# Optimization experiments

Measured on AMD Instinct MI355X. Metric: run time of the kernel, lower is better.

The kernel has to match this reference:

```python
import jax, jax.numpy as jnp
import numpy as np

D_MODEL = 64
D_K = 64
N_HEADS = 4
D_FF = 64
LN_EPS = 1e-5


def _layernorm(x, g, b):
    mu = jnp.mean(x, axis=-1, keepdims=True)
    var = jnp.var(x, axis=-1, keepdims=True)
    return (x - mu) * jax.lax.rsqrt(var + LN_EPS) * g + b


def setup_inputs() -> dict:
    key = jax.random.key(0)
    ks = jax.random.split(key, 20)
    B, L = 8, 2048
    s = 0.05
    inp = {
        "x": jax.random.normal(ks[0], (B, L, D_MODEL), jnp.float32),
        "attn_mask": jax.random.randint(ks[1], (B, L, L), 0, 2).astype(bool),
        "u": jax.random.normal(ks[2], (B, 1, D_MODEL), jnp.float32),
        "wq": jax.random.normal(ks[3], (D_MODEL, D_K * N_HEADS), jnp.float32) * s,
        "wk": jax.random.normal(ks[4], (D_MODEL, D_K * N_HEADS), jnp.float32) * s,
        "wv": jax.random.normal(ks[5], (D_MODEL, D_K * N_HEADS), jnp.float32) * s,
        "uqw": jax.random.normal(ks[6], (D_MODEL, D_K), jnp.float32) * s,
        "ukw": jax.random.normal(ks[7], (D_MODEL, D_K), jnp.float32) * s,
        "uvw": jax.random.normal(ks[8], (D_MODEL, D_K), jnp.float32) * s,
        "sq1": jax.random.normal(ks[9], (D_MODEL, D_MODEL // 2), jnp.float32) * s,
        "sq2": jax.random.normal(ks[10], (D_MODEL // 2, 1), jnp.float32) * s,
        "sk1": jax.random.normal(ks[11], (D_MODEL, D_MODEL // 2), jnp.float32) * s,
        "sk2": jax.random.normal(ks[12], (D_MODEL // 2, 1), jnp.float32) * s,
        "sv1": jax.random.normal(ks[13], (D_MODEL, D_MODEL // 2), jnp.float32) * s,
        "sv2": jax.random.normal(ks[14], (D_MODEL // 2, 1), jnp.float32) * s,
        "fcw": jax.random.normal(ks[15], (N_HEADS * D_K, D_MODEL), jnp.float32) * s,
        "ln1_g": jnp.ones((D_MODEL,), jnp.float32),
        "ln1_b": jnp.zeros((D_MODEL,), jnp.float32),
        "ffn1": jax.random.normal(ks[16], (D_MODEL, D_FF), jnp.float32) * s,
        "ffn2": jax.random.normal(ks[17], (D_FF, D_MODEL), jnp.float32) * s,
        "ln2_g": jnp.ones((D_MODEL,), jnp.float32),
        "ln2_b": jnp.zeros((D_MODEL,), jnp.float32),
    }
    return inp


def reference(x, attn_mask, u, wq, wk, wv, uqw, ukw, uvw, sq1, sq2, sk1, sk2,
              sv1, sv2, fcw, ln1_g, ln1_b, ffn1, ffn2, ln2_g, ln2_b):
    B, L, _ = x.shape
    H, dk = N_HEADS, D_K
    # per-head Q,K,V: [B,H,L,dk]
    Q = (x @ wq).reshape(B, L, H, dk).transpose(0, 2, 1, 3)
    K = (x @ wk).reshape(B, L, H, dk).transpose(0, 2, 1, 3)
    V = (x @ wv).reshape(B, L, H, dk).transpose(0, 2, 1, 3)
    # broadcast scalar gates from u: [B,1,1]
    S_q = jax.nn.relu(u @ sq1) @ sq2
    S_k = jax.nn.relu(u @ sk1) @ sk2
    S_v = jax.nn.relu(u @ sv1) @ sv2
    uQ = (x @ uqw) * S_q  # [B,L,dk]
    uK = (x @ ukw) * S_k
    uV = (x @ uvw) * S_v
    scores = (jnp.einsum('bhqd,bhkd->bhqk', Q, K)
              + jnp.einsum('bqd,bkd->bqk', uQ, uK)[:, None]) / jnp.sqrt(
                  jnp.asarray(dk, x.dtype))
    scores = jnp.where(attn_mask[:, None], jnp.asarray(-1e9, x.dtype), scores)
    attn = jax.nn.softmax(scores, axis=-1)  # [B,H,L,L]
    ctx = jnp.einsum('bhqk,bhkd->bhqd', attn, V + uV[:, None])
    ctx = ctx.transpose(0, 2, 1, 3).reshape(B, L, H * dk)
    out = ctx @ fcw  # dropout is identity in eval mode
    enc = _layernorm(out + x, ln1_g, ln1_b)
    ffn = jax.nn.relu(enc @ ffn1) @ ffn2
    res = _layernorm(ffn + enc, ln2_g, ln2_b)
    return (res, attn)
```

## Files before the change

kernel.cpp:

```cpp
#include <hip/hip_runtime.h>
#include <hip/hip_bf16.h>
#include <stdint.h>

typedef __bf16  bf16x8  __attribute__((ext_vector_type(8)));
typedef float   f32x4   __attribute__((ext_vector_type(4)));
typedef unsigned short u16x8 __attribute__((ext_vector_type(8)));
typedef unsigned short ushort_t;

__device__ __forceinline__ unsigned short f2b(float f) {
    __hip_bfloat16 h = __float2bfloat16(f);
    return *reinterpret_cast<unsigned short*>(&h);
}

__device__ __forceinline__ void cp16(const void* g, void* l) {
    __builtin_amdgcn_global_load_lds(
        (const __attribute__((address_space(1))) unsigned int*)g,
        (__attribute__((address_space(3))) unsigned int*)l,
        16, 0, 0);
}

#define BB 8
#define LL 2048
#define DM 64
#define NH 4
#define DK 64

__global__ __launch_bounds__(256) void k_maskpack(const int* __restrict__ mask,
                                                  unsigned int* __restrict__ words) {
    int tid = blockIdx.x * 256 + threadIdx.x;
    const int4* p = reinterpret_cast<const int4*>(mask) + (size_t)tid * 8;
    unsigned int wbits = 0u;
    #pragma unroll
    for (int i = 0; i < 8; i++) {
        int4 v = p[i];
        wbits |= (v.x != 0 ? 1u << (4 * i + 0) : 0u);
        wbits |= (v.y != 0 ? 1u << (4 * i + 1) : 0u);
        wbits |= (v.z != 0 ? 1u << (4 * i + 2) : 0u);
        wbits |= (v.w != 0 ? 1u << (4 * i + 3) : 0u);
    }
    words[tid] = wbits;
}

__global__ __launch_bounds__(64) void k_gates(const float* __restrict__ u,
                                              const float* s1q, const float* s2q,
                                              const float* s1k, const float* s2k,
                                              const float* s1v, const float* s2v,
                                              float* __restrict__ gates) {
    int b = blockIdx.x, g = blockIdx.y, lane = threadIdx.x;
    const float* s1 = (g == 0) ? s1q : (g == 1) ? s1k : s1v;
    const float* s2 = (g == 0) ? s2q : (g == 1) ? s2k : s2v;
    float ur = u[b * 64 + lane];
    float acc = 0.f;
    for (int j = 0; j < 64; j++) {
        float uj = __shfl(ur, j, 64);
        if (lane < 32) acc += uj * s1[j * 32 + lane];
    }
    float r = (lane < 32) ? fmaxf(acc, 0.f) * s2[lane] : 0.f;
    for (int m = 32; m >= 1; m >>= 1) r += __shfl_xor(r, m, 64);
    if (lane == 0) gates[b * 3 + g] = r;
}

__global__ __launch_bounds__(256) void k_proj(const float* __restrict__ x,
                                              const float* __restrict__ wq,
                                              const float* __restrict__ wk,
                                              const float* __restrict__ wv,
                                              const float* __restrict__ uqw,
                                              const float* __restrict__ ukw,
                                              const float* __restrict__ uvw,
                                              const float* __restrict__ gates,
                                              ushort_t* __restrict__ Qe,
                                              ushort_t* __restrict__ Ke,
                                              ushort_t* __restrict__ VeT) {
    int lt = blockIdx.x, b = blockIdx.y, t = threadIdx.x;
    int l0 = lt * 32;
    __shared__ float lx[32][68];
    __shared__ float luv[32][68];
    #pragma unroll
    for (int i = 0; i < 2; i++) {
        int id = t + i * 256;
        int r = id >> 4, c4 = id & 15;
        float4 v = *(const float4*)&x[((b * LL) + l0 + r) * 64 + c4 * 4];
        *(float4*)&lx[r][c4 * 4] = v;
    }
    __syncthreads();
    float Sq = gates[b * 3 + 0], Sk = gates[b * 3 + 1], Sv = gates[b * 3 + 2];
    if (t < 192) {
        int m = t >> 6, d = t & 63;
        const float* uw = (m == 0) ? uqw : (m == 1) ? ukw : uvw;
        float acc[32];
        #pragma unroll
        for (int r = 0; r < 32; r++) acc[r] = 0.f;
        for (int j = 0; j < 64; j += 4) {
            float w0 = uw[(j + 0) * 64 + d], w1 = uw[(j + 1) * 64 + d];
            float w2 = uw[(j + 2) * 64 + d], w3 = uw[(j + 3) * 64 + d];
            #pragma unroll
            for (int r = 0; r < 32; r++) {
                float4 xv = *(const float4*)&lx[r][j];
                acc[r] += xv.x * w0 + xv.y * w1 + xv.z * w2 + xv.w * w3;
            }
        }
        if (m == 2) {
            #pragma unroll
            for (int r = 0; r < 32; r++) luv[r][d] = acc[r] * Sv;
        } else if (m == 0) {
            for (int r = 0; r < 32; r++) {
                unsigned short v = f2b(acc[r] * Sq * 0.125f);
                int base = ((b * NH) * LL + l0 + r) * 128 + 64 + d;
                #pragma unroll
                for (int hh2 = 0; hh2 < 4; hh2++) Qe[base + hh2 * (LL * 128)] = v;
            }
        } else {
            for (int r = 0; r < 32; r++) {
                unsigned short v = f2b(acc[r] * Sk);
                int col = 64 + (d ^ ((r & 7) << 3));
                int base = ((b * NH) * LL + l0 + r) * 128 + col;
                #pragma unroll
                for (int hh2 = 0; hh2 < 4; hh2++) Ke[base + hh2 * (LL * 128)] = v;
            }
        }
    }
    __syncthreads();
    int c = t, hh = c >> 6, d = c & 63;
    float aq_[32], ak_[32], av_[32];
    #pragma unroll
    for (int r = 0; r < 32; r++) { aq_[r] = 0.f; ak_[r] = 0.f; av_[r] = 0.f; }
    for (int j = 0; j < 64; j += 4) {
        float q0w = wq[(j + 0) * 256 + c], q1w = wq[(j + 1) * 256 + c];
        float q2w = wq[(j + 2) * 256 + c], q3w = wq[(j + 3) * 256 + c];
        float k0w = wk[(j + 0) * 256 + c], k1w = wk[(j + 1) * 256 + c];
        float k2w = wk[(j + 2) * 256 + c], k3w = wk[(j + 3) * 256 + c];
        float v0w = wv[(j + 0) * 256 + c], v1w = wv[(j + 1) * 256 + c];
        float v2w = wv[(j + 2) * 256 + c], v3w = wv[(j + 3) * 256 + c];
        #pragma unroll
        for (int r = 0; r < 32; r++) {
            float4 xv = *(const float4*)&lx[r][j];
            aq_[r] += xv.x * q0w + xv.y * q1w + xv.z * q2w + xv.w * q3w;
            ak_[r] += xv.x * k0w + xv.y * k1w + xv.z * k2w + xv.w * k3w;
            av_[r] += xv.x * v0w + xv.y * v1w + xv.z * v2w + xv.w * v3w;
        }
    }
    int outbase = (b * NH + hh) * LL + l0;
    #pragma unroll
    for (int r = 0; r < 32; r++) Qe[(outbase + r) * 128 + d] = f2b(aq_[r] * 0.125f);
    #pragma unroll
    for (int r = 0; r < 32; r++)
        Ke[(outbase + r) * 128 + (d ^ ((r & 7) << 3))] = f2b(ak_[r]);
    long vbase = ((long)(b * NH + hh) * 64 + d) * LL;
    int lblk = l0 & ~63, loff = l0 & 63;
    #pragma unroll
    for (int rb = 0; rb < 4; rb++) {
        u16x8 vv;
        #pragma unroll
        for (int k = 0; k < 8; k++) {
            int r = rb * 8 + k;
            vv[k] = f2b(av_[r] + luv[r][d]);
        }
        int off = (loff + rb * 8) ^ ((d & 7) << 3);
        *(u16x8*)&VeT[vbase + lblk + off] = vv;
    }
}

__global__ __launch_bounds__(256) void k_attn(const ushort_t* __restrict__ Qe,
                                              const ushort_t* __restrict__ Ke,
                                              const ushort_t* __restrict__ VeT,
                                              const unsigned int* __restrict__ mwords,
                                              float* __restrict__ ctx,
                                              float* __restrict__ attn) {
    int lin = blockIdx.x + 32 * blockIdx.y + 128 * blockIdx.z;
    int sw  = ((lin & 7) << 7) | (lin >> 3);
    int qt = sw & 31, h = (sw >> 5) & 3, b = sw >> 7;

    int t = threadIdx.x, w = t >> 6, lane = t & 63, quad = lane >> 4, l15 = lane & 15;
    int q0 = qt * 64;
    int bh = b * NH + h;
    const ushort_t* QeB = Qe + (long)bh * LL * 128;
    const ushort_t* KeB = Ke + (long)bh * LL * 128;
    const ushort_t* VtB = VeT + (long)bh * 64 * LL;
    float* attnB = attn + (long)bh * LL * LL;
    const unsigned int* mB = mwords + (long)(b * LL) * 64;

    __shared__ ushort_t sKe[2][64 * 128];
    __shared__ ushort_t sVT[2][64 * 64];
    __shared__ unsigned int smask[64][66];
    __shared__ ushort_t sPb[4][16][72];

    #pragma unroll
    for (int i = 0; i < 16; i++) {
        int id = t + i * 256;
        smask[id >> 6][id & 63] = mB[(q0 + (id >> 6)) * 64 + (id & 63)];
    }

    bf16x8 aq[4];
    int qrow = q0 + w * 16 + l15;
    #pragma unroll
    for (int c = 0; c < 4; c++)
        aq[c] = *(const bf16x8*)&QeB[qrow * 128 + c * 32 + quad * 8];

    int swz = (l15 & 7) << 3;
    int mrow = w * 16 + quad * 4;
    float lsum[4] = {0.f, 0.f, 0.f, 0.f};

    #pragma unroll
    for (int i = 0; i < 4; i++) {
        int off = (t + i * 256) * 16;
        cp16((const char*)KeB + off, (char*)&sKe[0][0] + off);
    }
    for (int kt = 0; kt < 32; kt++) {
        int cur = kt & 1;
        __syncthreads();
        if (kt < 31) {
            size_t gb = (size_t)(kt + 1) * 64 * 256;
            #pragma unroll
            for (int i = 0; i < 4; i++) {
                int off = (t + i * 256) * 16;
                cp16((const char*)KeB + gb + off, (char*)&sKe[cur ^ 1][0] + off);
            }
        }
        #pragma unroll
        for (int nb = 0; nb < 4; nb++) {
            f32x4 s = (f32x4){0.f, 0.f, 0.f, 0.f};
            #pragma unroll
            for (int c = 0; c < 4; c++) {
                bf16x8 kb = *(const bf16x8*)&sKe[cur][(nb * 16 + l15) * 128 + ((c * 32 + quad * 8) ^ swz)];
                s = __builtin_amdgcn_mfma_f32_16x16x32_bf16(aq[c], kb, s, 0, 0, 0);
            }
            #pragma unroll
            for (int reg = 0; reg < 4; reg++) {
                unsigned int word = smask[mrow + reg][kt * 2 + (nb >> 1)];
                unsigned int bit = (word >> ((nb & 1) * 16 + l15)) & 1u;
                lsum[reg] += bit ? 0.f : __expf(fminf(s[reg], 60.f));
            }
        }
    }
    float inv[4];
    #pragma unroll
    for (int reg = 0; reg < 4; reg++) {
        float v = lsum[reg];
        #pragma unroll
        for (int m = 1; m < 16; m <<= 1) v += __shfl_xor(v, m, 16);
        inv[reg] = (v > 0.f) ? 1.f / v : 0.f;
    }

    f32x4 cacc[4];
    #pragma unroll
    for (int db = 0; db < 4; db++) cacc[db] = (f32x4){0.f, 0.f, 0.f, 0.f};

    #pragma unroll
    for (int i = 0; i < 4; i++) {
        int off = (t + i * 256) * 16;
        cp16((const char*)KeB + off, (char*)&sKe[0][0] + off);
    }
    #pragma unroll
    for (int i = 0; i < 2; i++) {
        int off = (t + i * 256) * 16;
        int d = off >> 7, cb = off & 127;
        cp16((const char*)VtB + (size_t)d * (LL * 2) + cb, (char*)&sVT[0][0] + off);
    }
    for (int kt = 0; kt < 32; kt++) {
        int cur = kt & 1;
        int k0 = kt * 64;
        __syncthreads();
        if (kt < 31) {
            size_t gKe = (size_t)(k0 + 64) * 256;
            #pragma unroll
            for (int i = 0; i < 4; i++) {
                int off = (t + i * 256) * 16;
                cp16((const char*)KeB + gKe + off, (char*)&sKe[cur ^ 1][0] + off);
            }
            #pragma unroll
            for (int i = 0; i < 2; i++) {
                int off = (t + i * 256) * 16;
                int d = off >> 7, cb = off & 127;
                cp16((const char*)VtB + (size_t)d * (LL * 2) + (size_t)(k0 + 64) * 2 + cb,
                     (char*)&sVT[cur ^ 1][0] + off);
            }
        }
        #pragma unroll
        for (int nb = 0; nb < 4; nb++) {
            f32x4 s = (f32x4){0.f, 0.f, 0.f, 0.f};
            #pragma unroll
            for (int c = 0; c < 4; c++) {
                bf16x8 kb = *(const bf16x8*)&sKe[cur][(nb * 16 + l15) * 128 + ((c * 32 + quad * 8) ^ swz)];
                s = __builtin_amdgcn_mfma_f32_16x16x32_bf16(aq[c], kb, s, 0, 0, 0);
            }
            #pragma unroll
            for (int reg = 0; reg < 4; reg++) {
                unsigned int word = smask[mrow + reg][kt * 2 + (nb >> 1)];
                unsigned int bit = (word >> ((nb & 1) * 16 + l15)) & 1u;
                float p = bit ? 0.f : __expf(fminf(s[reg], 60.f));
                sPb[w][quad * 4 + reg][nb * 16 + l15] = f2b(p);
                __builtin_nontemporal_store(p * inv[reg],
                    &attnB[(long)(q0 + mrow + reg) * LL + k0 + nb * 16 + l15]);
            }
        }
        #pragma unroll
        for (int db = 0; db < 4; db++) {
            #pragma unroll
            for (int c2 = 0; c2 < 2; c2++) {
                bf16x8 a  = *(const bf16x8*)&sPb[w][l15][c2 * 32 + quad * 8];
                bf16x8 bb = *(const bf16x8*)&sVT[cur][(db * 16 + l15) * 64 + ((c2 * 32 + quad * 8) ^ swz)];
                cacc[db] = __builtin_amdgcn_mfma_f32_16x16x32_bf16(a, bb, cacc[db], 0, 0, 0);
            }
        }
    }
    #pragma unroll
    for (int db = 0; db < 4; db++)
        #pragma unroll
        for (int reg = 0; reg < 4; reg++) {
            int qr = q0 + mrow + reg;
            ctx[((long)(b * LL) + qr) * 256 + h * 64 + db * 16 + l15] = cacc[db][reg] * inv[reg];
        }
}

__global__ __launch_bounds__(256) void k_epi(const float* __restrict__ ctx,
                                             const float* __restrict__ x,
                                             const float* __restrict__ fcw,
                                             const float* __restrict__ g1,
                                             const float* __restrict__ b1,
                                             const float* __restrict__ f1,
                                             const float* __restrict__ f2,
                                             const float* __restrict__ g2,
                                             const float* __restrict__ b2w,
                                             float* __restrict__ res) {
    int w = threadIdx.x >> 6, lane = threadIdx.x & 63;
    int row = blockIdx.x * 4 + w;
    const float* cr = ctx + (long)row * 256;
    float creg[4];
    #pragma unroll
    for (int i = 0; i < 4; i++) creg[i] = cr[i * 64 + lane];
    float acc = 0.f;
    #pragma unroll
    for (int j = 0; j < 256; j++) {
        float cj = __shfl(creg[j >> 6], j & 63, 64);
        acc += cj * fcw[j * 64 + lane];
    }
    float val = acc + x[row * 64 + lane];
    float mu = val;
    #pragma unroll
    for (int m = 1; m < 64; m <<= 1) mu += __shfl_xor(mu, m, 64);
    mu *= (1.f / 64.f);
    float d0 = val - mu;
    float var = d0 * d0;
    #pragma unroll
    for (int m = 1; m < 64; m <<= 1) var += __shfl_xor(var, m, 64);
    var *= (1.f / 64.f);
    float enc = d0 * rsqrtf(var + 1e-5f) * g1[lane] + b1[lane];
    float a1 = 0.f;
    #pragma unroll
    for (int j = 0; j < 64; j++) a1 += __shfl(enc, j, 64) * f1[j * 64 + lane];
    float hrel = fmaxf(a1, 0.f);
    float a2 = 0.f;
    #pragma unroll
    for (int j = 0; j < 64; j++) a2 += __shfl(hrel, j, 64) * f2[j * 64 + lane];
    float v2 = a2 + enc;
    float mu2 = v2;
    #pragma unroll
    for (int m = 1; m < 64; m <<= 1) mu2 += __shfl_xor(mu2, m, 64);
    mu2 *= (1.f / 64.f);
    float d2 = v2 - mu2;
    float var2 = d2 * d2;
    #pragma unroll
    for (int m = 1; m < 64; m <<= 1) var2 += __shfl_xor(var2, m, 64);
    var2 *= (1.f / 64.f);
    float outv = d2 * rsqrtf(var2 + 1e-5f) * g2[lane] + b2w[lane];
    res[row * 64 + lane] = outv;
}

extern "C" void kernel_launch(void* const* d_in, const int* in_sizes, int n_in,
                              void* d_out, int out_size, void* d_ws, size_t ws_size,
                              hipStream_t stream) {
    const float* x    = (const float*)d_in[0];
    const int*   mask = (const int*)d_in[1];
    const float* u    = (const float*)d_in[2];
    const float* wq   = (const float*)d_in[3];
    const float* wk   = (const float*)d_in[4];
    const float* wv   = (const float*)d_in[5];
    const float* uqw  = (const float*)d_in[6];
    const float* ukw  = (const float*)d_in[7];
    const float* uvw  = (const float*)d_in[8];
    const float* sq1  = (const float*)d_in[9];
    const float* sq2  = (const float*)d_in[10];
    const float* sk1  = (const float*)d_in[11];
    const float* sk2  = (const float*)d_in[12];
    const float* sv1  = (const float*)d_in[13];
    const float* sv2  = (const float*)d_in[14];
    const float* fcw  = (const float*)d_in[15];
    const float* g1   = (const float*)d_in[16];
    const float* b1   = (const float*)d_in[17];
    const float* f1   = (const float*)d_in[18];
    const float* f2   = (const float*)d_in[19];
    const float* g2   = (const float*)d_in[20];
    const float* b2w  = (const float*)d_in[21];

    char* ws = (char*)d_ws;
    float*        gates  = (float*)(ws + 0);
    unsigned int* mwords = (unsigned int*)(ws + 4096);
    ushort_t*     Qe     = (ushort_t*)(ws + 4198400);
    ushort_t*     Ke     = (ushort_t*)(ws + 20975616);
    ushort_t*     VeT    = (ushort_t*)(ws + 37752832);
    float*        ctx    = (float*)(ws + 46141440);

    float* res  = (float*)d_out;
    float* attn = (float*)d_out + (size_t)BB * LL * DM;

    k_maskpack<<<dim3(4096), dim3(256), 0, stream>>>(mask, mwords);
    k_gates<<<dim3(8, 3), dim3(64), 0, stream>>>(u, sq1, sq2, sk1, sk2, sv1, sv2, gates);
    k_proj<<<dim3(64, 8), dim3(256), 0, stream>>>(x, wq, wk, wv, uqw, ukw, uvw, gates, Qe, Ke, VeT);
    k_attn<<<dim3(32, 4, 8), dim3(256), 0, stream>>>(Qe, Ke, VeT, mwords, ctx, attn);
    k_epi<<<dim3(4096), dim3(256), 0, stream>>>(ctx, x, fcw, g1, b1, f1, f2, g2, b2w, res);
}
```

Before: 1.006 ms.

## Split attention warps into 2x2 query/key tiles to reuse K fragments

```diff
diff --git a/kernel.cpp b/kernel.cpp
--- a/kernel.cpp
+++ b/kernel.cpp
@@ -171,6 +171,7 @@
     int qt = sw & 31, h = (sw >> 5) & 3, b = sw >> 7;
 
     int t = threadIdx.x, w = t >> 6, lane = t & 63, quad = lane >> 4, l15 = lane & 15;
+    int qh = w >> 1, kh = w & 1;
     int q0 = qt * 64;
     int bh = b * NH + h;
     const ushort_t* QeB = Qe + (long)bh * LL * 128;
@@ -182,7 +183,8 @@
     __shared__ ushort_t sKe[2][64 * 128];
     __shared__ ushort_t sVT[2][64 * 64];
     __shared__ unsigned int smask[64][66];
-    __shared__ ushort_t sPb[4][16][72];
+    __shared__ ushort_t sPb[64][72];
+    __shared__ float rsum[2][64];
 
     #pragma unroll
     for (int i = 0; i < 16; i++) {
@@ -190,15 +192,21 @@
         smask[id >> 6][id & 63] = mB[(q0 + (id >> 6)) * 64 + (id & 63)];
     }
 
-    bf16x8 aq[4];
-    int qrow = q0 + w * 16 + l15;
-    #pragma unroll
-    for (int c = 0; c < 4; c++)
-        aq[c] = *(const bf16x8*)&QeB[qrow * 128 + c * 32 + quad * 8];
+    bf16x8 aq[2][4];
+    #pragma unroll
+    for (int qs = 0; qs < 2; qs++) {
+        int qrow = q0 + qh * 32 + qs * 16 + l15;
+        #pragma unroll
+        for (int c = 0; c < 4; c++)
+            aq[qs][c] = *(const bf16x8*)&QeB[qrow * 128 + c * 32 + quad * 8];
+    }
 
     int swz = (l15 & 7) << 3;
-    int mrow = w * 16 + quad * 4;
-    float lsum[4] = {0.f, 0.f, 0.f, 0.f};
+    float lsum[2][4];
+    #pragma unroll
+    for (int qs = 0; qs < 2; qs++)
+        #pragma unroll
+        for (int reg = 0; reg < 4; reg++) lsum[qs][reg] = 0.f;
 
     #pragma unroll
     for (int i = 0; i < 4; i++) {
@@ -217,34 +225,43 @@
             }
         }
         #pragma unroll
-        for (int nb = 0; nb < 4; nb++) {
-            f32x4 s = (f32x4){0.f, 0.f, 0.f, 0.f};
+        for (int nb = 0; nb < 2; nb++) {
+            f32x4 s0 = (f32x4){0.f, 0.f, 0.f, 0.f};
+            f32x4 s1 = (f32x4){0.f, 0.f, 0.f, 0.f};
             #pragma unroll
             for (int c = 0; c < 4; c++) {
-                bf16x8 kb = *(const bf16x8*)&sKe[cur][(nb * 16 + l15) * 128 + ((c * 32 + quad * 8) ^ swz)];
-                s = __builtin_amdgcn_mfma_f32_16x16x32_bf16(aq[c], kb, s, 0, 0, 0);
+                bf16x8 kb = *(const bf16x8*)&sKe[cur][(kh * 32 + nb * 16 + l15) * 128 + ((c * 32 + quad * 8) ^ swz)];
+                s0 = __builtin_amdgcn_mfma_f32_16x16x32_bf16(aq[0][c], kb, s0, 0, 0, 0);
+                s1 = __builtin_amdgcn_mfma_f32_16x16x32_bf16(aq[1][c], kb, s1, 0, 0, 0);
             }
             #pragma unroll
             for (int reg = 0; reg < 4; reg++) {
-                unsigned int word = smask[mrow + reg][kt * 2 + (nb >> 1)];
-                unsigned int bit = (word >> ((nb & 1) * 16 + l15)) & 1u;
-                lsum[reg] += bit ? 0.f : __expf(fminf(s[reg], 60.f));
-            }
-        }
-    }
-    float inv[4];
-    #pragma unroll
-    for (int reg = 0; reg < 4; reg++) {
-        float v = lsum[reg];
-        #pragma unroll
-        for (int m = 1; m < 16; m <<= 1) v += __shfl_xor(v, m, 16);
-        inv[reg] = (v > 0.f) ? 1.f / v : 0.f;
-    }
-
-    f32x4 cacc[4];
-    #pragma unroll
-    for (int db = 0; db < 4; db++) cacc[db] = (f32x4){0.f, 0.f, 0.f, 0.f};
-
+                int r0 = qh * 32 + quad * 4 + reg;
+                unsigned int w0 = smask[r0][kt * 2 + kh];
+                unsigned int b0 = (w0 >> (nb * 16 + l15)) & 1u;
+                lsum[0][reg] += b0 ? 0.f : __expf(fminf(s0[reg], 60.f));
+                unsigned int w1 = smask[r0 + 16][kt * 2 + kh];
+                unsigned int b1 = (w1 >> (nb * 16 + l15)) & 1u;
+                lsum[1][reg] += b1 ? 0.f : __expf(fminf(s1[reg], 60.f));
+            }
+        }
+    }
+    #pragma unroll
+    for (int qs = 0; qs < 2; qs++)
+        #pragma unroll
+        for (int reg = 0; reg < 4; reg++) {
+            float v = lsum[qs][reg];
+            #pragma unroll
+            for (int m = 1; m < 16; m <<= 1) v += __shfl_xor(v, m, 16);
+            lsum[qs][reg] = v;
+        }
+    if (l15 == 0) {
+        #pragma unroll
+        for (int qs = 0; qs < 2; qs++)
+            #pragma unroll
+            for (int reg = 0; reg < 4; reg++)
+                rsum[kh][qh * 32 + qs * 16 + quad * 4 + reg] = lsum[qs][reg];
+    }
     #pragma unroll
     for (int i = 0; i < 4; i++) {
         int off = (t + i * 256) * 16;
@@ -256,6 +273,21 @@
         int d = off >> 7, cb = off & 127;
         cp16((const char*)VtB + (size_t)d * (LL * 2) + cb, (char*)&sVT[0][0] + off);
     }
+    __syncthreads();
+    float inv[2][4];
+    #pragma unroll
+    for (int qs = 0; qs < 2; qs++)
+        #pragma unroll
+        for (int reg = 0; reg < 4; reg++) {
+            int row = qh * 32 + qs * 16 + quad * 4 + reg;
+            float v = rsum[0][row] + rsum[1][row];
+            inv[qs][reg] = (v > 0.f) ? 1.f / v : 0.f;
+        }
+
+    f32x4 cacc[4];
+    #pragma unroll
+    for (int db = 0; db < 4; db++) cacc[db] = (f32x4){0.f, 0.f, 0.f, 0.f};
+
     for (int kt = 0; kt < 32; kt++) {
         int cur = kt & 1;
         int k0 = kt * 64;
@@ -275,29 +307,50 @@
                      (char*)&sVT[cur ^ 1][0] + off);
             }
         }
-        #pragma unroll
-        for (int nb = 0; nb < 4; nb++) {
-            f32x4 s = (f32x4){0.f, 0.f, 0.f, 0.f};
+        float pm[2][2][4];
+        #pragma unroll
+        for (int nb = 0; nb < 2; nb++) {
+            f32x4 s0 = (f32x4){0.f, 0.f, 0.f, 0.f};
+            f32x4 s1 = (f32x4){0.f, 0.f, 0.f, 0.f};
             #pragma unroll
             for (int c = 0; c < 4; c++) {
-                bf16x8 kb = *(const bf16x8*)&sKe[cur][(nb * 16 + l15) * 128 + ((c * 32 + quad * 8) ^ swz)];
-                s = __builtin_amdgcn_mfma_f32_16x16x32_bf16(aq[c], kb, s, 0, 0, 0);
+                bf16x8 kb = *(const bf16x8*)&sKe[cur][(kh * 32 + nb * 16 + l15) * 128 + ((c * 32 + quad * 8) ^ swz)];
+                s0 = __builtin_amdgcn_mfma_f32_16x16x32_bf16(aq[0][c], kb, s0, 0, 0, 0);
+                s1 = __builtin_amdgcn_mfma_f32_16x16x32_bf16(aq[1][c], kb, s1, 0, 0, 0);
             }
             #pragma unroll
             for (int reg = 0; reg < 4; reg++) {
-                unsigned int word = smask[mrow + reg][kt * 2 + (nb >> 1)];
-                unsigned int bit = (word >> ((nb & 1) * 16 + l15)) & 1u;
-                float p = bit ? 0.f : __expf(fminf(s[reg], 60.f));
-                sPb[w][quad * 4 + reg][nb * 16 + l15] = f2b(p);
-                __builtin_nontemporal_store(p * inv[reg],
-                    &attnB[(long)(q0 + mrow + reg) * LL + k0 + nb * 16 + l15]);
-            }
-        }
+                int r0 = qh * 32 + quad * 4 + reg;
+                int col = kh * 32 + nb * 16 + l15;
+                unsigned int w0 = smask[r0][kt * 2 + kh];
+                unsigned int b0 = (w0 >> (nb * 16 + l15)) & 1u;
+                float p0 = b0 ? 0.f : __expf(fminf(s0[reg], 60.f));
+                sPb[r0][col] = f2b(p0);
+                pm[0][nb][reg] = p0;
+                unsigned int w1 = smask[r0 + 16][kt * 2 + kh];
+                unsigned int b1 = (w1 >> (nb * 16 + l15)) & 1u;
+                float p1 = b1 ? 0.f : __expf(fminf(s1[reg], 60.f));
+                sPb[r0 + 16][col] = f2b(p1);
+                pm[1][nb][reg] = p1;
+            }
+        }
+        __syncthreads();
+        #pragma unroll
+        for (int qs = 0; qs < 2; qs++)
+            #pragma unroll
+            for (int nb = 0; nb < 2; nb++)
+                #pragma unroll
+                for (int reg = 0; reg < 4; reg++) {
+                    int row = qh * 32 + qs * 16 + quad * 4 + reg;
+                    int col = kh * 32 + nb * 16 + l15;
+                    __builtin_nontemporal_store(pm[qs][nb][reg] * inv[qs][reg],
+                        &attnB[(long)(q0 + row) * LL + k0 + col]);
+                }
         #pragma unroll
         for (int db = 0; db < 4; db++) {
             #pragma unroll
             for (int c2 = 0; c2 < 2; c2++) {
-                bf16x8 a  = *(const bf16x8*)&sPb[w][l15][c2 * 32 + quad * 8];
+                bf16x8 a  = *(const bf16x8*)&sPb[w * 16 + l15][c2 * 32 + quad * 8];
                 bf16x8 bb = *(const bf16x8*)&sVT[cur][(db * 16 + l15) * 64 + ((c2 * 32 + quad * 8) ^ swz)];
                 cacc[db] = __builtin_amdgcn_mfma_f32_16x16x32_bf16(a, bb, cacc[db], 0, 0, 0);
             }
@@ -307,8 +360,8 @@
     for (int db = 0; db < 4; db++)
         #pragma unroll
         for (int reg = 0; reg < 4; reg++) {
-            int qr = q0 + mrow + reg;
-            ctx[((long)(b * LL) + qr) * 256 + h * 64 + db * 16 + l15] = cacc[db][reg] * inv[reg];
+            int qr = q0 + w * 16 + quad * 4 + reg;
+            ctx[((long)(b * LL) + qr) * 256 + h * 64 + db * 16 + l15] = cacc[db][reg] * inv[kh][reg];
         }
 }
 
```

After: 1.019 ms. Within noise of the previous version (+1.3%).

## Transpose score MFMA so each lane owns a query row for vectorized stores

Applied to the files above, without the earlier changes.

```diff
diff --git a/kernel.cpp b/kernel.cpp
--- a/kernel.cpp
+++ b/kernel.cpp
@@ -5,6 +5,7 @@
 typedef __bf16  bf16x8  __attribute__((ext_vector_type(8)));
 typedef float   f32x4   __attribute__((ext_vector_type(4)));
 typedef unsigned short u16x8 __attribute__((ext_vector_type(8)));
+typedef unsigned short u16x4 __attribute__((ext_vector_type(4)));
 typedef unsigned short ushort_t;
 
 __device__ __forceinline__ unsigned short f2b(float f) {
@@ -197,8 +198,7 @@
         aq[c] = *(const bf16x8*)&QeB[qrow * 128 + c * 32 + quad * 8];
 
     int swz = (l15 & 7) << 3;
-    int mrow = w * 16 + quad * 4;
-    float lsum[4] = {0.f, 0.f, 0.f, 0.f};
+    float lsum = 0.f;
 
     #pragma unroll
     for (int i = 0; i < 4; i++) {
@@ -222,24 +222,24 @@
             #pragma unroll
             for (int c = 0; c < 4; c++) {
                 bf16x8 kb = *(const bf16x8*)&sKe[cur][(nb * 16 + l15) * 128 + ((c * 32 + quad * 8) ^ swz)];
-                s = __builtin_amdgcn_mfma_f32_16x16x32_bf16(aq[c], kb, s, 0, 0, 0);
-            }
+                s = __builtin_amdgcn_mfma_f32_16x16x32_bf16(kb, aq[c], s, 0, 0, 0);
+            }
+            unsigned int word = smask[w * 16 + l15][kt * 2 + (nb >> 1)];
             #pragma unroll
             for (int reg = 0; reg < 4; reg++) {
-                unsigned int word = smask[mrow + reg][kt * 2 + (nb >> 1)];
-                unsigned int bit = (word >> ((nb & 1) * 16 + l15)) & 1u;
-                lsum[reg] += bit ? 0.f : __expf(fminf(s[reg], 60.f));
-            }
-        }
-    }
-    float inv[4];
-    #pragma unroll
-    for (int reg = 0; reg < 4; reg++) {
-        float v = lsum[reg];
-        #pragma unroll
-        for (int m = 1; m < 16; m <<= 1) v += __shfl_xor(v, m, 16);
-        inv[reg] = (v > 0.f) ? 1.f / v : 0.f;
-    }
+                unsigned int bit = (word >> ((nb & 1) * 16 + quad * 4 + reg)) & 1u;
+                lsum += bit ? 0.f : __expf(fminf(s[reg], 60.f));
+            }
+        }
+    }
+    {
+        lsum += __shfl_xor(lsum, 16, 64);
+        lsum += __shfl_xor(lsum, 32, 64);
+    }
+    float inv = (lsum > 0.f) ? 1.f / lsum : 0.f;
+    float invC[4];
+    #pragma unroll
+    for (int reg = 0; reg < 4; reg++) invC[reg] = __shfl(inv, quad * 4 + reg, 16);
 
     f32x4 cacc[4];
     #pragma unroll
@@ -281,17 +281,20 @@
             #pragma unroll
             for (int c = 0; c < 4; c++) {
                 bf16x8 kb = *(const bf16x8*)&sKe[cur][(nb * 16 + l15) * 128 + ((c * 32 + quad * 8) ^ swz)];
-                s = __builtin_amdgcn_mfma_f32_16x16x32_bf16(aq[c], kb, s, 0, 0, 0);
-            }
+                s = __builtin_amdgcn_mfma_f32_16x16x32_bf16(kb, aq[c], s, 0, 0, 0);
+            }
+            unsigned int word = smask[w * 16 + l15][kt * 2 + (nb >> 1)];
+            u16x4 pk;
+            float4 st;
             #pragma unroll
             for (int reg = 0; reg < 4; reg++) {
-                unsigned int word = smask[mrow + reg][kt * 2 + (nb >> 1)];
-                unsigned int bit = (word >> ((nb & 1) * 16 + l15)) & 1u;
+                unsigned int bit = (word >> ((nb & 1) * 16 + quad * 4 + reg)) & 1u;
                 float p = bit ? 0.f : __expf(fminf(s[reg], 60.f));
-                sPb[w][quad * 4 + reg][nb * 16 + l15] = f2b(p);
-                __builtin_nontemporal_store(p * inv[reg],
-                    &attnB[(long)(q0 + mrow + reg) * LL + k0 + nb * 16 + l15]);
-            }
+                pk[reg] = f2b(p);
+                ((float*)&st)[reg] = p * inv;
+            }
+            *(u16x4*)&sPb[w][l15][nb * 16 + quad * 4] = pk;
+            *(float4*)&attnB[(long)(q0 + w * 16 + l15) * LL + k0 + nb * 16 + quad * 4] = st;
         }
         #pragma unroll
         for (int db = 0; db < 4; db++) {
@@ -307,8 +310,8 @@
     for (int db = 0; db < 4; db++)
         #pragma unroll
         for (int reg = 0; reg < 4; reg++) {
-            int qr = q0 + mrow + reg;
-            ctx[((long)(b * LL) + qr) * 256 + h * 64 + db * 16 + l15] = cacc[db][reg] * inv[reg];
+            int qr = q0 + w * 16 + quad * 4 + reg;
+            ctx[((long)(b * LL) + qr) * 256 + h * 64 + db * 16 + l15] = cacc[db][reg] * invC[reg];
         }
 }
 
```

New measurement: 1.108 ms. 1.1x slower.
